# Kernel optimization log

Hardware: AMD Instinct MI355X
Metric: run time of the kernel (lower is better)

Reference implementation:

```python
import jax, jax.numpy as jnp
import numpy as np

B, T, N = 512, 1024, 50
ROOT_IDX, END_IDX = 0, 1
NEG_INF = -10000.0


def setup_inputs() -> dict:
    key = jax.random.key(0)
    k1, k2, k3, k4 = jax.random.split(key, 4)
    input_features = jax.random.normal(k1, (B, T, N), dtype=jnp.float32)
    # xavier_uniform on [N, N]: bound = sqrt(6 / (N + N))
    bound = float(np.sqrt(6.0 / (N + N)))
    log_transitions = jax.random.uniform(k2, (N, N), minval=-bound, maxval=bound, dtype=jnp.float32)
    log_transitions = log_transitions.at[:, ROOT_IDX].set(NEG_INF)
    log_transitions = log_transitions.at[END_IDX, :].set(NEG_INF)
    target_tags = jax.random.randint(k3, (B, T), 0, N).astype(jnp.int64)
    # contiguous prefix mask from random lengths in [T//2, T]
    lengths = jax.random.randint(k4, (B,), T // 2, T + 1)
    input_mask = (jnp.arange(T)[None, :] < lengths[:, None]).astype(jnp.int32)
    return {
        "input_features": input_features,
        "log_transitions": log_transitions,
        "target_tags": target_tags,
        "input_mask": input_mask,
    }


def _crf_nll(input_features, log_transitions, target_tags, input_mask):
    maskf = input_mask.astype(input_features.dtype)  # [B, T]

    # ---- forward belief propagation (log partition) ----
    alpha0 = log_transitions[ROOT_IDX, :][None, :] + input_features[:, 0, :]  # [B, N]
    feats_t = jnp.swapaxes(input_features, 0, 1)  # [T, B, N]
    mask_t = jnp.swapaxes(maskf, 0, 1)            # [T, B]

    def step(alpha, xs):
        feat, m = xs  # [B, N], [B]
        # next_tag_var[b, i, j] = alpha[b, i] + feat[b, j] + trans[i, j]
        nxt = alpha[:, :, None] + feat[:, None, :] + log_transitions[None, :, :]
        new = jax.nn.logsumexp(nxt, axis=1)  # [B, N]
        m = m[:, None]
        return new * m + alpha * (1.0 - m), None

    alpha, _ = jax.lax.scan(step, alpha0, (feats_t[1:], mask_t[1:]))
    log_z = jax.nn.logsumexp(alpha + log_transitions[:, END_IDX][None, :], axis=-1)  # [B]

    # ---- gold sequence score (vectorized over time) ----
    tags = target_tags  # [B, T]
    scores = log_transitions[ROOT_IDX, tags[:, 0]]  # [B]
    # per-position emission score of the gold tag
    emis = jnp.take_along_axis(input_features, tags[:, :, None], axis=2)[:, :, 0]  # [B, T]
    trans = log_transitions[tags[:, :-1], tags[:, 1:]]  # [B, T-1]
    scores = scores + jnp.sum(trans * maskf[:, 1:], axis=1) + jnp.sum(emis[:, :-1] * maskf[:, :-1], axis=1)
    last_idx = jnp.sum(input_mask, axis=1) - 1  # [B]
    last_tags = jnp.take_along_axis(tags, last_idx[:, None], axis=1)[:, 0]  # [B]
    last_emit = jnp.take_along_axis(input_features[:, -1, :], last_tags[:, None], axis=1)[:, 0]
    scores = scores + log_transitions[last_tags, END_IDX] + last_emit * maskf[:, -1]

    return log_z - scores  # negative log likelihood, [B]


def reference(input_features, log_transitions, target_tags, input_mask):
    return _crf_nll(input_features, log_transitions, target_tags, input_mask)
```

## Files before the change

### kernel.cpp

```cpp
#include <hip/hip_runtime.h>
#include <math.h>

#define BB 512
#define TT 1024
#define NS 50
#define LCOLS 33

typedef _Float16 half2_t __attribute__((ext_vector_type(2)));

static __device__ __forceinline__ half2_t pk_h2(float a, float b) {
    auto r = __builtin_amdgcn_cvt_pkrtz(a, b);
    return __builtin_bit_cast(half2_t, r);
}
static __device__ __forceinline__ float wave_sum_f(float v) {
    #pragma unroll
    for (int k = 32; k >= 1; k >>= 1) v += __shfl_xor(v, k, 64);
    return v;
}
static __device__ __forceinline__ int wave_sum_i(int v) {
    #pragma unroll
    for (int k = 32; k >= 1; k >>= 1) v += __shfl_xor(v, k, 64);
    return v;
}
#define FDOT(a, b, c) __builtin_amdgcn_fdot2((a), (b), (c), false)

__global__ __launch_bounds__(128, 1) void crf_nll_kernel(
    const float* __restrict__ feat,
    const float* __restrict__ trans,
    const int*   __restrict__ tags,
    const int*   __restrict__ mask,
    float* __restrict__ out)
{
    const int b    = blockIdx.x;
    const int tid  = threadIdx.x;
    const int w    = tid >> 6;
    const int lane = tid & 63;
    const int jj   = (lane < NS) ? lane : 0;

    __shared__ float sh_comb[64];
    __shared__ float sh_sc[2];
    __shared__ int   sh_Kb;
    __shared__ float lds[2][2][NS * LCOLS];

#define INIT_E(m) half2_t e##m; { \
        int r0 = w ? (jj * NS + 2*(m)) : ((2*(m)) * NS + jj); \
        int r1 = r0 + (w ? 1 : NS); \
        float x0 = __expf(trans[r0]); \
        float x1 = __expf(trans[r1]); \
        if (lane >= NS) { x0 = 0.f; x1 = 0.f; } \
        e##m = pk_h2(x0, x1); }
    INIT_E(0)  INIT_E(1)  INIT_E(2)  INIT_E(3)  INIT_E(4)
    INIT_E(5)  INIT_E(6)  INIT_E(7)  INIT_E(8)  INIT_E(9)
    INIT_E(10) INIT_E(11) INIT_E(12) INIT_E(13) INIT_E(14)
    INIT_E(15) INIT_E(16) INIT_E(17) INIT_E(18) INIT_E(19)
    INIT_E(20) INIT_E(21) INIT_E(22) INIT_E(23) INIT_E(24)
#undef INIT_E

    int cnt = 0;
    for (int t = lane; t < TT; t += 64) cnt += mask[b * TT + t];
    const int len = wave_sum_i(cnt);
    const int tm  = (len - 1) >> 1;
    const int nst = w ? (len - 1 - tm) : tm;

    const float* fb = feat + (size_t)b * TT * NS;

    float u;
    if (w == 0) u = (lane < NS) ? __expf(trans[jj] + fb[jj]) : 0.f;
    else        u = (lane < NS) ? __expf(trans[jj * NS + 1] + fb[(size_t)(len - 1) * NS + jj]) : 0.f;
    int K = 0, kp, rlp;
    { int bb2 = __builtin_amdgcn_readlane(__float_as_int(u), 7);
      kp = ((bb2 >> 23) & 255) - 127; }
    rlp = 0x3F800000;

    auto step = [&](float eexp) {
        kp += ((rlp >> 23) & 255) - 127;
        K  += kp;
        int rr = (127 - kp) << 23;
        float p = u * __int_as_float(rr);
        rlp = __builtin_amdgcn_readlane(__float_as_int(p), 7);
        int pn_ = __builtin_amdgcn_update_dpp(
            __float_as_int(p), __float_as_int(p), 0xB1, 0xF, 0xF, true);
        float pnf = __int_as_float(pn_);
        half2_t pk = pk_h2(p, pnf);
        int pki = __builtin_bit_cast(int, pk);
        int r0_  = __builtin_amdgcn_readlane(pki, 0);
        int r1_  = __builtin_amdgcn_readlane(pki, 2);
        int r2_  = __builtin_amdgcn_readlane(pki, 4);
        int r3_  = __builtin_amdgcn_readlane(pki, 6);
        int r4_  = __builtin_amdgcn_readlane(pki, 8);
        int r5_  = __builtin_amdgcn_readlane(pki, 10);
        int r6_  = __builtin_amdgcn_readlane(pki, 12);
        int r7_  = __builtin_amdgcn_readlane(pki, 14);
        int r8_  = __builtin_amdgcn_readlane(pki, 16);
        int r9_  = __builtin_amdgcn_readlane(pki, 18);
        int r10_ = __builtin_amdgcn_readlane(pki, 20);
        int r11_ = __builtin_amdgcn_readlane(pki, 22);
        int r12_ = __builtin_amdgcn_readlane(pki, 24);
        int r13_ = __builtin_amdgcn_readlane(pki, 26);
        int r14_ = __builtin_amdgcn_readlane(pki, 28);
        int r15_ = __builtin_amdgcn_readlane(pki, 30);
        int r16_ = __builtin_amdgcn_readlane(pki, 32);
        int r17_ = __builtin_amdgcn_readlane(pki, 34);
        int r18_ = __builtin_amdgcn_readlane(pki, 36);
        int r19_ = __builtin_amdgcn_readlane(pki, 38);
        int r20_ = __builtin_amdgcn_readlane(pki, 40);
        int r21_ = __builtin_amdgcn_readlane(pki, 42);
        int r22_ = __builtin_amdgcn_readlane(pki, 44);
        int r23_ = __builtin_amdgcn_readlane(pki, 46);
        int r24_ = __builtin_amdgcn_readlane(pki, 48);
        __builtin_amdgcn_sched_barrier(0);
        float s0 = 0.f, s1 = 0.f, s2 = 0.f, s3 = 0.f;
        float s4 = 0.f, s5 = 0.f, s6 = 0.f, s7 = 0.f;
#define FD(r, em, acc) acc = FDOT(__builtin_bit_cast(half2_t, r), em, acc);
        FD(r0_,  e0,  s0) FD(r1_,  e1,  s1) FD(r2_,  e2,  s2) FD(r3_,  e3,  s3)
        FD(r4_,  e4,  s4) FD(r5_,  e5,  s5) FD(r6_,  e6,  s6) FD(r7_,  e7,  s7)
        FD(r8_,  e8,  s0) FD(r9_,  e9,  s1) FD(r10_, e10, s2) FD(r11_, e11, s3)
        FD(r12_, e12, s4) FD(r13_, e13, s5) FD(r14_, e14, s6) FD(r15_, e15, s7)
        FD(r16_, e16, s0) FD(r17_, e17, s1) FD(r18_, e18, s2) FD(r19_, e19, s3)
        FD(r20_, e20, s4) FD(r21_, e21, s5) FD(r22_, e22, s6) FD(r23_, e23, s7)
        FD(r24_, e24, s0)
#undef FD
        float S = ((s0 + s1) + (s2 + s3)) + ((s4 + s5) + (s6 + s7));
        u = S * eexp;
    };

    auto chunk_base = [&](int cs) -> int {
        int bs = w ? (len - 33 - 32 * cs) : (1 + 32 * cs);
        return bs < 0 ? 0 : bs;
    };

    float2 g0, g1, g2, g3, g4, g5, g6, g7, g8, g9, g10, g11, g12;
    g12.x = 0.f; g12.y = 0.f;
    auto issue_loads = [&](int cs) {
        int base = chunk_base(cs);
        const float2* gp = (const float2*)(fb + (size_t)base * NS);
        g0  = gp[0*64  + lane];  g1  = gp[1*64  + lane];
        g2  = gp[2*64  + lane];  g3  = gp[3*64  + lane];
        g4  = gp[4*64  + lane];  g5  = gp[5*64  + lane];
        g6  = gp[6*64  + lane];  g7  = gp[7*64  + lane];
        g8  = gp[8*64  + lane];  g9  = gp[9*64  + lane];
        g10 = gp[10*64 + lane];  g11 = gp[11*64 + lane];
        if (lane < 32) g12 = gp[12*64 + lane];
    };
    auto exp_write = [&](int cs, float* L) {
        int base = chunk_base(cs);
        int LD2  = len - 2 - 32 * cs;
#define WR(gi, i) { \
        int d   = (i) * 128 + lane * 2; \
        int r   = d / 50; \
        int col = d - r * 50; \
        int sr  = w ? (LD2 - (base + r)) : r; \
        bool ok = (((i) < 12) || (lane < 32)) && (sr >= 0) && (sr < 32); \
        if (ok) { L[col * LCOLS + sr]       = __expf(gi.x); \
                  L[(col + 1) * LCOLS + sr] = __expf(gi.y); } }
        WR(g0,0)  WR(g1,1)  WR(g2,2)  WR(g3,3)  WR(g4,4)  WR(g5,5)
        WR(g6,6)  WR(g7,7)  WR(g8,8)  WR(g9,9)  WR(g10,10) WR(g11,11)
        WR(g12,12)
#undef WR
    };

    float c0, c1, c2, c3, c4, c5, c6, c7;
    auto prime = [&](const float* L) {
        const float* Lp = L + jj * LCOLS;
        c0 = Lp[0]; c1 = Lp[1]; c2 = Lp[2]; c3 = Lp[3];
        c4 = Lp[4]; c5 = Lp[5]; c6 = Lp[6]; c7 = Lp[7];
    };

    const int nfull = nst >> 5;
    const int tail  = nst & 31;

    issue_loads(0);
    exp_write(0, &lds[w][0][0]);
    issue_loads(1);
    __asm__ volatile("s_waitcnt lgkmcnt(0)" ::: "memory");
    __builtin_amdgcn_sched_barrier(0);
    prime(&lds[w][0][0]);

    int bufc = 0;
    for (int c = 0; c < nfull; ++c) {
        const float* L  = &lds[w][bufc][0] + jj * LCOLS;
        #pragma unroll 1
        for (int it = 0; it < 4; ++it) {
            int nidx = ((it + 1) * 8) & 31;
            float n0 = L[nidx + 0], n1 = L[nidx + 1], n2 = L[nidx + 2], n3 = L[nidx + 3];
            float n4 = L[nidx + 4], n5 = L[nidx + 5], n6 = L[nidx + 6], n7 = L[nidx + 7];
            step(c0); step(c1); step(c2); step(c3);
            step(c4); step(c5); step(c6); step(c7);
            c0 = n0; c1 = n1; c2 = n2; c3 = n3;
            c4 = n4; c5 = n5; c6 = n6; c7 = n7;
        }
        float* Lnxt = &lds[w][bufc ^ 1][0];
        exp_write(c + 1, Lnxt);
        issue_loads(c + 2);
        __asm__ volatile("s_waitcnt lgkmcnt(0)" ::: "memory");
        __builtin_amdgcn_sched_barrier(0);
        prime(Lnxt);
        bufc ^= 1;
    }

    if (tail) {
        const float* L = &lds[w][bufc][0] + jj * LCOLS;
        int rem = tail;
        #pragma unroll 1
        for (int it = 0; it < 4 && rem > 0; ++it) {
            int nidx = ((it + 1) * 8) & 31;
            float n0 = L[nidx + 0], n1 = L[nidx + 1], n2 = L[nidx + 2], n3 = L[nidx + 3];
            float n4 = L[nidx + 4], n5 = L[nidx + 5], n6 = L[nidx + 6], n7 = L[nidx + 7];
            if (rem > 0) { step(c0); --rem; }
            if (rem > 0) { step(c1); --rem; }
            if (rem > 0) { step(c2); --rem; }
            if (rem > 0) { step(c3); --rem; }
            if (rem > 0) { step(c4); --rem; }
            if (rem > 0) { step(c5); --rem; }
            if (rem > 0) { step(c6); --rem; }
            if (rem > 0) { step(c7); --rem; }
            c0 = n0; c1 = n1; c2 = n2; c3 = n3;
            c4 = n4; c5 = n5; c6 = n6; c7 = n7;
        }
    }

    if (w == 1) {
        sh_comb[lane] = u * __expf(-fb[(size_t)tm * NS + jj]);
        if (lane == 0) sh_Kb = K;
    }

    const int* tb = tags + (size_t)b * TT;
    float sc = 0.0f;
    for (int t2 = tid; t2 < len; t2 += 128) {
        int tg = tb[t2];
        sc += fb[(size_t)t2 * NS + tg];
        if (t2 >= 1) sc += trans[tb[t2 - 1] * NS + tg];
    }
    sc = wave_sum_f(sc);
    if (lane == 0) sh_sc[w] = sc;

    __syncthreads();

    if (w == 0) {
        float wv = u * sh_comb[lane];
        float W = wave_sum_f(wv);
        float log_z = __logf(W) + (float)(K + sh_Kb) * 0.6931471805599453f;
        if (lane == 0) {
            float sct = sh_sc[0] + sh_sc[1]
                      + trans[tb[0]]
                      + trans[tb[len - 1] * NS + 1];
            out[b] = log_z - sct;
        }
    }
}

extern "C" void kernel_launch(void* const* d_in, const int* in_sizes, int n_in,
                              void* d_out, int out_size, void* d_ws, size_t ws_size,
                              hipStream_t stream) {
    const float* feat  = (const float*)d_in[0];
    const float* trans = (const float*)d_in[1];
    const int*   tags  = (const int*)d_in[2];
    const int*   mask  = (const int*)d_in[3];
    float* out = (float*)d_out;
    crf_nll_kernel<<<dim3(BB), dim3(128), 0, stream>>>(feat, trans, tags, mask, out);
}
```

Measured before the change: 271.1 us.

## Pack four sequences per block with smaller LDS chunks and per-step rescale

Each block now handles four batch sequences (512 threads) instead of one, and the launch is reduced to BB/4 blocks. The LDS staging chunk shrinks from 32 to 16 time steps to fit four sequences' double buffers. The rescaling exponent is now computed at the end of each step from the new u rather than lagging one step. This aims to improve occupancy and latency hiding for the serial forward recursion, but it doubles chunk-refill synchronization points and adds a readlane on the critical path of each step.

```diff
diff --git a/kernel.cpp b/kernel.cpp
--- a/kernel.cpp
+++ b/kernel.cpp
@@ -4,7 +4,9 @@
 #define BB 512
 #define TT 1024
 #define NS 50
-#define LCOLS 33
+#define SPB 4
+#define CH 16
+#define LCOLS 17
 
 typedef _Float16 half2_t __attribute__((ext_vector_type(2)));
 
@@ -24,23 +26,24 @@
 }
 #define FDOT(a, b, c) __builtin_amdgcn_fdot2((a), (b), (c), false)
 
-__global__ __launch_bounds__(128, 1) void crf_nll_kernel(
+__global__ __launch_bounds__(512, 2) void crf_nll_kernel(
     const float* __restrict__ feat,
     const float* __restrict__ trans,
     const int*   __restrict__ tags,
     const int*   __restrict__ mask,
     float* __restrict__ out)
 {
-    const int b    = blockIdx.x;
     const int tid  = threadIdx.x;
-    const int w    = tid >> 6;
+    const int s    = tid >> 7;
+    const int w    = (tid >> 6) & 1;
     const int lane = tid & 63;
     const int jj   = (lane < NS) ? lane : 0;
-
-    __shared__ float sh_comb[64];
-    __shared__ float sh_sc[2];
-    __shared__ int   sh_Kb;
-    __shared__ float lds[2][2][NS * LCOLS];
+    const int b    = blockIdx.x * SPB + s;
+
+    __shared__ float sh_comb[SPB][64];
+    __shared__ float sh_sc[SPB][2];
+    __shared__ int   sh_Kb[SPB];
+    __shared__ float lds[SPB][2][2][NS * LCOLS];
 
 #define INIT_E(m) half2_t e##m; { \
         int r0 = w ? (jj * NS + 2*(m)) : ((2*(m)) * NS + jj); \
@@ -67,17 +70,13 @@
     float u;
     if (w == 0) u = (lane < NS) ? __expf(trans[jj] + fb[jj]) : 0.f;
     else        u = (lane < NS) ? __expf(trans[jj * NS + 1] + fb[(size_t)(len - 1) * NS + jj]) : 0.f;
-    int K = 0, kp, rlp;
+    int K = 0, kp, rr;
     { int bb2 = __builtin_amdgcn_readlane(__float_as_int(u), 7);
-      kp = ((bb2 >> 23) & 255) - 127; }
-    rlp = 0x3F800000;
+      kp = ((bb2 >> 23) & 255) - 127; rr = (127 - kp) << 23; }
 
     auto step = [&](float eexp) {
-        kp += ((rlp >> 23) & 255) - 127;
-        K  += kp;
-        int rr = (127 - kp) << 23;
+        K += kp;
         float p = u * __int_as_float(rr);
-        rlp = __builtin_amdgcn_readlane(__float_as_int(p), 7);
         int pn_ = __builtin_amdgcn_update_dpp(
             __float_as_int(p), __float_as_int(p), 0xB1, 0xF, 0xF, true);
         float pnf = __int_as_float(pn_);
@@ -122,40 +121,38 @@
 #undef FD
         float S = ((s0 + s1) + (s2 + s3)) + ((s4 + s5) + (s6 + s7));
         u = S * eexp;
+        int bb2 = __builtin_amdgcn_readlane(__float_as_int(u), 7);
+        kp = ((bb2 >> 23) & 255) - 127;
+        rr = (127 - kp) << 23;
     };
 
     auto chunk_base = [&](int cs) -> int {
-        int bs = w ? (len - 33 - 32 * cs) : (1 + 32 * cs);
+        int bs = w ? (len - (CH + 1) - CH * cs) : (1 + CH * cs);
         return bs < 0 ? 0 : bs;
     };
 
-    float2 g0, g1, g2, g3, g4, g5, g6, g7, g8, g9, g10, g11, g12;
-    g12.x = 0.f; g12.y = 0.f;
+    float2 g0, g1, g2, g3, g4, g5, g6;
+    g6.x = 0.f; g6.y = 0.f;
     auto issue_loads = [&](int cs) {
         int base = chunk_base(cs);
         const float2* gp = (const float2*)(fb + (size_t)base * NS);
-        g0  = gp[0*64  + lane];  g1  = gp[1*64  + lane];
-        g2  = gp[2*64  + lane];  g3  = gp[3*64  + lane];
-        g4  = gp[4*64  + lane];  g5  = gp[5*64  + lane];
-        g6  = gp[6*64  + lane];  g7  = gp[7*64  + lane];
-        g8  = gp[8*64  + lane];  g9  = gp[9*64  + lane];
-        g10 = gp[10*64 + lane];  g11 = gp[11*64 + lane];
-        if (lane < 32) g12 = gp[12*64 + lane];
+        g0 = gp[0*64 + lane];  g1 = gp[1*64 + lane];
+        g2 = gp[2*64 + lane];  g3 = gp[3*64 + lane];
+        g4 = gp[4*64 + lane];  g5 = gp[5*64 + lane];
+        if (lane < 16) g6 = gp[6*64 + lane];
     };
     auto exp_write = [&](int cs, float* L) {
         int base = chunk_base(cs);
-        int LD2  = len - 2 - 32 * cs;
+        int LD2  = len - 2 - CH * cs;
 #define WR(gi, i) { \
         int d   = (i) * 128 + lane * 2; \
         int r   = d / 50; \
         int col = d - r * 50; \
         int sr  = w ? (LD2 - (base + r)) : r; \
-        bool ok = (((i) < 12) || (lane < 32)) && (sr >= 0) && (sr < 32); \
+        bool ok = (((i) < 6) || (lane < 16)) && (sr >= 0) && (sr < CH); \
         if (ok) { L[col * LCOLS + sr]       = __expf(gi.x); \
                   L[(col + 1) * LCOLS + sr] = __expf(gi.y); } }
-        WR(g0,0)  WR(g1,1)  WR(g2,2)  WR(g3,3)  WR(g4,4)  WR(g5,5)
-        WR(g6,6)  WR(g7,7)  WR(g8,8)  WR(g9,9)  WR(g10,10) WR(g11,11)
-        WR(g12,12)
+        WR(g0,0) WR(g1,1) WR(g2,2) WR(g3,3) WR(g4,4) WR(g5,5) WR(g6,6)
 #undef WR
     };
 
@@ -166,22 +163,22 @@
         c4 = Lp[4]; c5 = Lp[5]; c6 = Lp[6]; c7 = Lp[7];
     };
 
-    const int nfull = nst >> 5;
-    const int tail  = nst & 31;
+    const int nfull = nst >> 4;
+    const int tail  = nst & 15;
 
     issue_loads(0);
-    exp_write(0, &lds[w][0][0]);
+    exp_write(0, &lds[s][w][0][0]);
     issue_loads(1);
     __asm__ volatile("s_waitcnt lgkmcnt(0)" ::: "memory");
     __builtin_amdgcn_sched_barrier(0);
-    prime(&lds[w][0][0]);
+    prime(&lds[s][w][0][0]);
 
     int bufc = 0;
     for (int c = 0; c < nfull; ++c) {
-        const float* L  = &lds[w][bufc][0] + jj * LCOLS;
+        const float* L  = &lds[s][w][bufc][0] + jj * LCOLS;
         #pragma unroll 1
-        for (int it = 0; it < 4; ++it) {
-            int nidx = ((it + 1) * 8) & 31;
+        for (int it = 0; it < 2; ++it) {
+            int nidx = ((it + 1) * 8) & 15;
             float n0 = L[nidx + 0], n1 = L[nidx + 1], n2 = L[nidx + 2], n3 = L[nidx + 3];
             float n4 = L[nidx + 4], n5 = L[nidx + 5], n6 = L[nidx + 6], n7 = L[nidx + 7];
             step(c0); step(c1); step(c2); step(c3);
@@ -189,7 +186,7 @@
             c0 = n0; c1 = n1; c2 = n2; c3 = n3;
             c4 = n4; c5 = n5; c6 = n6; c7 = n7;
         }
-        float* Lnxt = &lds[w][bufc ^ 1][0];
+        float* Lnxt = &lds[s][w][bufc ^ 1][0];
         exp_write(c + 1, Lnxt);
         issue_loads(c + 2);
         __asm__ volatile("s_waitcnt lgkmcnt(0)" ::: "memory");
@@ -199,11 +196,11 @@
     }
 
     if (tail) {
-        const float* L = &lds[w][bufc][0] + jj * LCOLS;
+        const float* L = &lds[s][w][bufc][0] + jj * LCOLS;
         int rem = tail;
         #pragma unroll 1
-        for (int it = 0; it < 4 && rem > 0; ++it) {
-            int nidx = ((it + 1) * 8) & 31;
+        for (int it = 0; it < 2 && rem > 0; ++it) {
+            int nidx = ((it + 1) * 8) & 15;
             float n0 = L[nidx + 0], n1 = L[nidx + 1], n2 = L[nidx + 2], n3 = L[nidx + 3];
             float n4 = L[nidx + 4], n5 = L[nidx + 5], n6 = L[nidx + 6], n7 = L[nidx + 7];
             if (rem > 0) { step(c0); --rem; }
@@ -220,28 +217,28 @@
     }
 
     if (w == 1) {
-        sh_comb[lane] = u * __expf(-fb[(size_t)tm * NS + jj]);
-        if (lane == 0) sh_Kb = K;
+        sh_comb[s][lane] = u * __expf(-fb[(size_t)tm * NS + jj]);
+        if (lane == 0) sh_Kb[s] = K;
     }
 
     const int* tb = tags + (size_t)b * TT;
     float sc = 0.0f;
-    for (int t2 = tid; t2 < len; t2 += 128) {
+    for (int t2 = w * 64 + lane; t2 < len; t2 += 128) {
         int tg = tb[t2];
         sc += fb[(size_t)t2 * NS + tg];
         if (t2 >= 1) sc += trans[tb[t2 - 1] * NS + tg];
     }
     sc = wave_sum_f(sc);
-    if (lane == 0) sh_sc[w] = sc;
+    if (lane == 0) sh_sc[s][w] = sc;
 
     __syncthreads();
 
     if (w == 0) {
-        float wv = u * sh_comb[lane];
+        float wv = u * sh_comb[s][lane];
         float W = wave_sum_f(wv);
-        float log_z = __logf(W) + (float)(K + sh_Kb) * 0.6931471805599453f;
+        float log_z = __logf(W) + (float)(K + sh_Kb[s]) * 0.6931471805599453f;
         if (lane == 0) {
-            float sct = sh_sc[0] + sh_sc[1]
+            float sct = sh_sc[s][0] + sh_sc[s][1]
                       + trans[tb[0]]
                       + trans[tb[len - 1] * NS + 1];
             out[b] = log_z - sct;
@@ -257,5 +254,5 @@
     const int*   tags  = (const int*)d_in[2];
     const int*   mask  = (const int*)d_in[3];
     float* out = (float*)d_out;
-    crf_nll_kernel<<<dim3(BB), dim3(128), 0, stream>>>(feat, trans, tags, mask, out);
-}
+    crf_nll_kernel<<<dim3(BB / SPB), dim3(512), 0, stream>>>(feat, trans, tags, mask, out);
+}
```

Result: slower. 283.2 us (+4.5%).
